# Optimization experiments

Hardware: AMD Instinct MI355X
Metric: run time of the kernel (lower is better)

## Reference

```python
import jax, jax.numpy as jnp
import numpy as np

N = 50000   # num_nodes
E = 600000  # num_edges
F = 128     # num_features
H = 128     # hidden_dim
C = 40      # num_classes


def setup_inputs() -> dict:
    key = jax.random.key(0)
    ks = jax.random.split(key, 8)
    x = jax.random.normal(ks[0], (N, F), dtype=jnp.float32)
    edge_index = jax.random.randint(ks[1], (2, E), 0, N, dtype=jnp.int64)
    # alpha predictors (torch inits these to zero; use small random so alpha is non-trivial)
    aw1 = jax.random.normal(ks[2], (F, 1), dtype=jnp.float32) * 0.01
    ab1 = jnp.zeros((1,), dtype=jnp.float32)
    aw2 = jax.random.normal(ks[3], (H, 1), dtype=jnp.float32) * 0.01
    ab2 = jnp.zeros((1,), dtype=jnp.float32)
    # projection weights, torch layout [out, in], xavier-uniform-ish scale
    W1 = jax.random.normal(ks[4], (H, F), dtype=jnp.float32) * np.sqrt(2.0 / (F + H))
    b1 = jnp.zeros((H,), dtype=jnp.float32)
    W2 = jax.random.normal(ks[5], (C, H), dtype=jnp.float32) * np.sqrt(2.0 / (H + C))
    b2 = jnp.zeros((C,), dtype=jnp.float32)
    return {"x": x, "edge_index": edge_index, "aw1": aw1, "ab1": ab1,
            "W1": W1, "b1": b1, "aw2": aw2, "ab2": ab2, "W2": W2, "b2": b2}


def _gso_edges(edge_index):
    """Add self loops and compute GCN-normalized edge weights: D^-1/2 (A+I) D^-1/2."""
    loops = jnp.arange(N, dtype=edge_index.dtype)
    row = jnp.concatenate([edge_index[0], loops])
    col = jnp.concatenate([edge_index[1], loops])
    deg = jax.ops.segment_sum(jnp.ones(row.shape, dtype=jnp.float32), row, num_segments=N)
    dinv = jnp.where(deg > 0, jax.lax.rsqrt(deg), 0.0)
    w = dinv[row] * dinv[col]  # [E+N]
    return row, col, w


def _layer(x, row, col, w, aw, ab, Wt, b, activate):
    alpha = jax.nn.sigmoid(x @ aw + ab)                              # [N,1]
    z_lp = jax.ops.segment_sum(w[:, None] * x[col], row, num_segments=N)  # S_LP @ x
    z_hp = x - z_lp                                                  # S_HP = I - S_LP
    z = alpha * z_lp + (1.0 - alpha) * z_hp
    out = z @ Wt.T + b
    return jax.nn.relu(out) if activate else out


def reference(x, edge_index, aw1, ab1, W1, b1, aw2, ab2, W2, b2):
    row, col, w = _gso_edges(edge_index)
    h = _layer(x, row, col, w, aw1, ab1, W1, b1, True)   # dropout p in eval = identity
    out = _layer(h, row, col, w, aw2, ab2, W2, b2, False)
    return out
```

## Files before the change

kernel.cpp:

```cpp
#include <hip/hip_runtime.h>

#define F 128
#define BIN_CAP 6144

typedef _Float16 half8 __attribute__((ext_vector_type(8)));
typedef float f32x4 __attribute__((ext_vector_type(4)));

__device__ inline unsigned int f2_to_h2(float a, float b) {
    union { _Float16 h[2]; unsigned int u; } c;
    c.h[0] = (_Float16)a; c.h[1] = (_Float16)b;
    return c.u;
}
__device__ inline float2 h2_to_f2(unsigned int v) {
    union { unsigned int u; _Float16 h[2]; } c; c.u = v;
    return make_float2((float)c.h[0], (float)c.h[1]);
}

__global__ void zc_kernel(int* __restrict__ binCnt, const float* __restrict__ x,
                          const float* __restrict__ W1, const float* __restrict__ W2,
                          unsigned int* __restrict__ xf, unsigned int* __restrict__ w1f,
                          unsigned int* __restrict__ w2f, int nx) {
    int i = blockIdx.x * blockDim.x + threadIdx.x;
    if (i < 256) { binCnt[i] = 0; return; }
    int j = i - 256;
    if (j < nx) {
        float2 v = ((const float2*)x)[j];
        xf[j] = f2_to_h2(v.x, v.y);
    } else if (j < nx + (F * F / 2)) {
        int k = j - nx;
        float2 v = ((const float2*)W1)[k];
        w1f[k] = f2_to_h2(v.x, v.y);
    } else if (j < nx + (F * F / 2) + (48 * F / 2)) {
        int k = j - nx - (F * F / 2);
        int m = k >> 6;
        if (m < 40) {
            float2 v = ((const float2*)W2)[k];
            w2f[k] = f2_to_h2(v.x, v.y);
        } else {
            w2f[k] = 0u;
        }
    }
}

__global__ __launch_bounds__(256) void binning_kernel(const int* __restrict__ row,
                                                      const int* __restrict__ col,
                                                      int* __restrict__ binCnt,
                                                      unsigned int* __restrict__ binned, int e) {
    __shared__ int cnt1[256], base[256], cnt2[256];
    int chunk0 = blockIdx.x * 4096;
    cnt1[threadIdx.x] = 0;
    cnt2[threadIdx.x] = 0;
    __syncthreads();
    #pragma unroll
    for (int k = 0; k < 16; ++k) {
        int i = chunk0 + k * 256 + threadIdx.x;
        if (i < e) atomicAdd(&cnt1[row[i] >> 8], 1);
    }
    __syncthreads();
    int c = cnt1[threadIdx.x];
    if (c > 0) base[threadIdx.x] = atomicAdd(&binCnt[threadIdx.x], c);
    __syncthreads();
    #pragma unroll
    for (int k = 0; k < 16; ++k) {
        int i = chunk0 + k * 256 + threadIdx.x;
        if (i < e) {
            int r = row[i], cl = col[i];
            int b = r >> 8;
            int rk = atomicAdd(&cnt2[b], 1);
            int pos = base[b] + rk;
            if (pos < BIN_CAP)
                binned[(size_t)b * BIN_CAP + pos] = ((unsigned int)(r & 255) << 24) | (unsigned int)cl;
        }
    }
}

__global__ __launch_bounds__(256) void finalize_kernel(const int* __restrict__ binCnt,
                                                       const unsigned int* __restrict__ binned,
                                                       int* __restrict__ rowStart,
                                                       float* __restrict__ dinv,
                                                       int* __restrict__ csr_col,
                                                       int n, int nb) {
    __shared__ int tmp[256], lc[256], lo[256], lc2[256];
    __shared__ int sBase, sSz;
    int tid = threadIdx.x;
    int b = blockIdx.x;
    int v = (tid < nb) ? binCnt[tid] : 0;
    tmp[tid] = v;
    __syncthreads();
    #pragma unroll
    for (int off = 1; off < 256; off <<= 1) {
        int t = (tid >= off) ? tmp[tid - off] : 0;
        __syncthreads();
        tmp[tid] += t;
        __syncthreads();
    }
    if (tid == b) { sBase = tmp[b] - v; sSz = v; }
    lc[tid] = 0;
    lc2[tid] = 0;
    __syncthreads();
    int base = sBase, sz = sSz;
    for (int i = tid; i < sz; i += 256) {
        unsigned int pv = binned[(size_t)b * BIN_CAP + i];
        atomicAdd(&lc[pv >> 24], 1);
    }
    __syncthreads();
    int cv = lc[tid];
    tmp[tid] = cv;
    __syncthreads();
    #pragma unroll
    for (int off = 1; off < 256; off <<= 1) {
        int t = (tid >= off) ? tmp[tid - off] : 0;
        __syncthreads();
        tmp[tid] += t;
        __syncthreads();
    }
    int myLo = tmp[tid] - cv;
    lo[tid] = myLo;
    int rowId = (b << 8) + tid;
    if (rowId < n) {
        rowStart[rowId] = base + myLo;
        dinv[rowId] = rsqrtf((float)(cv + 1));
    }
    if (tid == 0 && b == nb - 1) rowStart[n] = base + sz;
    __syncthreads();
    for (int i = tid; i < sz; i += 256) {
        unsigned int pv = binned[(size_t)b * BIN_CAP + i];
        int rl = pv >> 24;
        int rk = atomicAdd(&lc2[rl], 1);
        csr_col[base + lo[rl] + rk] = (int)(pv & 0xFFFFFFu);
    }
}

__global__ void gather_kernel(const unsigned int* __restrict__ featf,
                              const int* __restrict__ rowStart, const int* __restrict__ csr_col,
                              const float* __restrict__ dinv, const float* __restrict__ aw,
                              const float* __restrict__ ab, unsigned int* __restrict__ zf, int n) {
    int wid = (blockIdx.x * blockDim.x + threadIdx.x) >> 6;
    int lane = threadIdx.x & 63;
    if (wid >= n) return;
    float2 xv = h2_to_f2(featf[(size_t)wid * 64 + lane]);
    float2 awv = ((const float2*)aw)[lane];
    float s = xv.x * awv.x + xv.y * awv.y;
    #pragma unroll
    for (int off = 32; off > 0; off >>= 1) s += __shfl_down(s, off);
    s = __shfl(s, 0);
    float a = 1.0f / (1.0f + expf(-(s + ab[0])));
    float dr = dinv[wid];
    float2 acc;
    acc.x = dr * dr * xv.x;
    acc.y = dr * dr * xv.y;
    int j = rowStart[wid], en = rowStart[wid + 1];
    for (; j + 3 < en; j += 4) {
        int c0 = csr_col[j], c1 = csr_col[j + 1], c2 = csr_col[j + 2], c3 = csr_col[j + 3];
        float w0 = dr * dinv[c0], w1 = dr * dinv[c1], w2 = dr * dinv[c2], w3 = dr * dinv[c3];
        float2 f0 = h2_to_f2(featf[(size_t)c0 * 64 + lane]);
        float2 f1 = h2_to_f2(featf[(size_t)c1 * 64 + lane]);
        float2 f2 = h2_to_f2(featf[(size_t)c2 * 64 + lane]);
        float2 f3 = h2_to_f2(featf[(size_t)c3 * 64 + lane]);
        acc.x += w0 * f0.x; acc.y += w0 * f0.y;
        acc.x += w1 * f1.x; acc.y += w1 * f1.y;
        acc.x += w2 * f2.x; acc.y += w2 * f2.y;
        acc.x += w3 * f3.x; acc.y += w3 * f3.y;
    }
    for (; j < en; ++j) {
        int c0 = csr_col[j];
        float w0 = dr * dinv[c0];
        float2 f0 = h2_to_f2(featf[(size_t)c0 * 64 + lane]);
        acc.x += w0 * f0.x; acc.y += w0 * f0.y;
    }
    float ca = 1.0f - a, cb = 2.0f * a - 1.0f;
    zf[(size_t)wid * 64 + lane] = f2_to_h2(ca * xv.x + cb * acc.x, ca * xv.y + cb * acc.y);
}

__global__ __launch_bounds__(256) void mfma_dense_kernel(
    const _Float16* __restrict__ zf, const _Float16* __restrict__ w1f,
    const float* __restrict__ b1, const float* __restrict__ aw2,
    const float* __restrict__ ab2, const _Float16* __restrict__ w2f,
    _Float16* __restrict__ yf, float* __restrict__ alpha2, int n) {
    __shared__ _Float16 hs[64 * F];
    int wv = threadIdx.x >> 6;
    int l = threadIdx.x & 63;
    int lr = l & 15;
    int kg = l >> 4;
    int node0 = blockIdx.x * 64;

    int arow = node0 + wv * 16 + lr;
    bool rowok = arow < n;
    half8 afr[4];
    half8 hzero = {0, 0, 0, 0, 0, 0, 0, 0};
    #pragma unroll
    for (int ks = 0; ks < 4; ++ks) {
        afr[ks] = rowok ? *(const half8*)(zf + (size_t)arow * F + ks * 32 + kg * 8) : hzero;
    }

    f32x4 acc[8];
    #pragma unroll
    for (int ct = 0; ct < 8; ++ct) {
        f32x4 a = {0.f, 0.f, 0.f, 0.f};
        #pragma unroll
        for (int ks = 0; ks < 4; ++ks) {
            half8 b = *(const half8*)(w1f + (size_t)(ct * 16 + lr) * F + ks * 32 + kg * 8);
            a = __builtin_amdgcn_mfma_f32_16x16x32_f16(afr[ks], b, a, 0, 0, 0);
        }
        acc[ct] = a;
    }

    float part[4] = {0.f, 0.f, 0.f, 0.f};
    #pragma unroll
    for (int ct = 0; ct < 8; ++ct) {
        int colc = ct * 16 + lr;
        float bv = b1[colc];
        float av = aw2[colc];
        #pragma unroll
        for (int r = 0; r < 4; ++r) {
            float h = fmaxf(acc[ct][r] + bv, 0.f);
            part[r] += h * av;
            int hrow = wv * 16 + kg * 4 + r;
            int byteoff = (hrow * 256 + colc * 2) ^ ((hrow & 7) << 4);
            *(_Float16*)((char*)hs + byteoff) = (_Float16)h;
        }
    }
    #pragma unroll
    for (int off = 1; off < 16; off <<= 1) {
        #pragma unroll
        for (int r = 0; r < 4; ++r) part[r] += __shfl_xor(part[r], off);
    }
    if (lr == 0) {
        #pragma unroll
        for (int r = 0; r < 4; ++r) {
            int nd = node0 + wv * 16 + kg * 4 + r;
            if (nd < n) alpha2[nd] = 1.0f / (1.0f + expf(-(part[r] + ab2[0])));
        }
    }
    __syncthreads();

    int hrow = wv * 16 + lr;
    half8 a2[4];
    #pragma unroll
    for (int ks = 0; ks < 4; ++ks) {
        int byteoff = (hrow * 256 + (ks * 32 + kg * 8) * 2) ^ ((hrow & 7) << 4);
        a2[ks] = *(const half8*)((char*)hs + byteoff);
    }
    #pragma unroll
    for (int ct = 0; ct < 3; ++ct) {
        f32x4 a = {0.f, 0.f, 0.f, 0.f};
        #pragma unroll
        for (int ks = 0; ks < 4; ++ks) {
            half8 b = *(const half8*)(w2f + (size_t)(ct * 16 + lr) * F + ks * 32 + kg * 8);
            a = __builtin_amdgcn_mfma_f32_16x16x32_f16(a2[ks], b, a, 0, 0, 0);
        }
        int colc = ct * 16 + lr;
        if (colc < 40) {
            #pragma unroll
            for (int r = 0; r < 4; ++r) {
                int nd = node0 + wv * 16 + kg * 4 + r;
                if (nd < n) yf[(size_t)nd * 40 + colc] = (_Float16)a[r];
            }
        }
    }
}

__global__ void gather40_kernel(const _Float16* __restrict__ yf,
                                const int* __restrict__ rowStart, const int* __restrict__ csr_col,
                                const float* __restrict__ dinv, const float* __restrict__ alpha,
                                const float* __restrict__ bias, float* __restrict__ out, int n) {
    int node = blockIdx.x * 8 + threadIdx.x / 40;
    int lane = threadIdx.x % 40;
    if (node >= n) return;
    float yv = (float)yf[(size_t)node * 40 + lane];
    float dr = dinv[node];
    float acc = dr * dr * yv;
    int j = rowStart[node], en = rowStart[node + 1];
    for (; j + 3 < en; j += 4) {
        int c0 = csr_col[j], c1 = csr_col[j + 1], c2 = csr_col[j + 2], c3 = csr_col[j + 3];
        acc += dr * dinv[c0] * (float)yf[(size_t)c0 * 40 + lane];
        acc += dr * dinv[c1] * (float)yf[(size_t)c1 * 40 + lane];
        acc += dr * dinv[c2] * (float)yf[(size_t)c2 * 40 + lane];
        acc += dr * dinv[c3] * (float)yf[(size_t)c3 * 40 + lane];
    }
    for (; j < en; ++j) {
        int c0 = csr_col[j];
        acc += dr * dinv[c0] * (float)yf[(size_t)c0 * 40 + lane];
    }
    float a = alpha[node];
    out[(size_t)node * 40 + lane] = (1.0f - a) * yv + (2.0f * a - 1.0f) * acc + bias[lane];
}

extern "C" void kernel_launch(void* const* d_in, const int* in_sizes, int n_in,
                              void* d_out, int out_size, void* d_ws, size_t ws_size,
                              hipStream_t stream) {
    const float* x   = (const float*)d_in[0];
    const int*   ei  = (const int*)d_in[1];
    const float* aw1 = (const float*)d_in[2];
    const float* ab1 = (const float*)d_in[3];
    const float* W1  = (const float*)d_in[4];
    const float* b1  = (const float*)d_in[5];
    const float* aw2 = (const float*)d_in[6];
    const float* ab2 = (const float*)d_in[7];
    const float* W2  = (const float*)d_in[8];
    const float* b2  = (const float*)d_in[9];
    float* out = (float*)d_out;

    int n = in_sizes[0] / F;
    int e = in_sizes[1] / 2;
    const int* row = ei;
    const int* col = ei + e;
    int nb = (n + 255) >> 8;

    char* p = (char*)d_ws;
    auto alloc = [&](size_t bytes) { char* q = p; p += (bytes + 15) & ~(size_t)15; return q; };
    int*   binCnt   = (int*)alloc(256 * 4);
    int*   rowStart = (int*)alloc((size_t)(n + 2) * 4);
    float* dinv     = (float*)alloc((size_t)n * 4);
    unsigned int* binned = (unsigned int*)alloc((size_t)nb * BIN_CAP * 4);
    int*   csr_col  = (int*)alloc((size_t)e * 4);
    unsigned int* w1f = (unsigned int*)alloc((size_t)F * F * 2);
    unsigned int* w2f = (unsigned int*)alloc((size_t)48 * F * 2);
    unsigned int* xf  = (unsigned int*)alloc((size_t)n * 64 * 4);
    unsigned int* zf  = (unsigned int*)alloc((size_t)n * 64 * 4);
    _Float16* yfbuf = (_Float16*)alloc((size_t)n * 40 * 2);
    float* alpha2   = (float*)alloc((size_t)n * 4);

    int nx = n * 64;

    int nzc = 256 + nx + (F * F / 2) + (48 * F / 2);
    zc_kernel<<<(nzc + 255) / 256, 256, 0, stream>>>(binCnt, x, W1, W2, xf, w1f, w2f, nx);

    binning_kernel<<<(e + 4095) / 4096, 256, 0, stream>>>(row, col, binCnt, binned, e);
    finalize_kernel<<<nb, 256, 0, stream>>>(binCnt, binned, rowStart, dinv, csr_col, n, nb);

    gather_kernel<<<(n + 3) / 4, 256, 0, stream>>>(xf, rowStart, csr_col, dinv,
                                                   aw1, ab1, zf, n);

    int gblk = (n + 63) / 64;
    mfma_dense_kernel<<<gblk, 256, 0, stream>>>((const _Float16*)zf, (const _Float16*)w1f,
                                                b1, aw2, ab2, (const _Float16*)w2f,
                                                yfbuf, alpha2, n);

    gather40_kernel<<<(n + 7) / 8, 320, 0, stream>>>(yfbuf, rowStart, csr_col, dinv,
                                                     alpha2, b2, out, n);
}
```

Measured before the change: 128.6 us.

## Split layer-1 gather into two feature-half passes and precompute alpha in convert

The conversion kernel now computes the layer-1 alpha gate per node while converting x to fp16, storing it in a new buffer. The layer-1 gather is split into two launches, each handling half of the feature columns with 32 lanes per node. Each pass touches only half of every neighbour row, so its working set is smaller and may fit the cache better for the random neighbour reads. The cost is re-reading the CSR indices and dinv twice and paying an extra kernel launch.

```diff
diff --git a/kernel.cpp b/kernel.cpp
--- a/kernel.cpp
+++ b/kernel.cpp
@@ -16,30 +16,42 @@
     return make_float2((float)c.h[0], (float)c.h[1]);
 }
 
-__global__ void zc_kernel(int* __restrict__ binCnt, const float* __restrict__ x,
-                          const float* __restrict__ W1, const float* __restrict__ W2,
-                          unsigned int* __restrict__ xf, unsigned int* __restrict__ w1f,
-                          unsigned int* __restrict__ w2f, int nx) {
-    int i = blockIdx.x * blockDim.x + threadIdx.x;
-    if (i < 256) { binCnt[i] = 0; return; }
-    int j = i - 256;
-    if (j < nx) {
-        float2 v = ((const float2*)x)[j];
-        xf[j] = f2_to_h2(v.x, v.y);
-    } else if (j < nx + (F * F / 2)) {
-        int k = j - nx;
-        float2 v = ((const float2*)W1)[k];
-        w1f[k] = f2_to_h2(v.x, v.y);
-    } else if (j < nx + (F * F / 2) + (48 * F / 2)) {
-        int k = j - nx - (F * F / 2);
-        int m = k >> 6;
-        if (m < 40) {
-            float2 v = ((const float2*)W2)[k];
-            w2f[k] = f2_to_h2(v.x, v.y);
+__global__ __launch_bounds__(256) void convert_kernel(
+    const float* __restrict__ x, const float* __restrict__ aw1, const float* __restrict__ ab1,
+    const float* __restrict__ W1, const float* __restrict__ W2,
+    unsigned int* __restrict__ xf, float* __restrict__ alpha1,
+    unsigned int* __restrict__ w1f, unsigned int* __restrict__ w2f,
+    int* __restrict__ binCnt, int n, int nodeBlocks) {
+    if (blockIdx.x >= nodeBlocks) {
+        int i = (blockIdx.x - nodeBlocks) * 256 + threadIdx.x;
+        if (i < 256) {
+            binCnt[i] = 0;
+        } else if (i < 256 + F * F / 2) {
+            int j = i - 256;
+            float2 v = ((const float2*)W1)[j];
+            w1f[j] = f2_to_h2(v.x, v.y);
         } else {
-            w2f[k] = 0u;
-        }
-    }
+            int j = i - 256 - F * F / 2;
+            int m = j >> 6;
+            if (m < 40) {
+                float2 v = ((const float2*)W2)[j];
+                w2f[j] = f2_to_h2(v.x, v.y);
+            } else {
+                w2f[j] = 0u;
+            }
+        }
+        return;
+    }
+    int wid = blockIdx.x * 4 + (threadIdx.x >> 6);
+    int lane = threadIdx.x & 63;
+    if (wid >= n) return;
+    float2 xv = ((const float2*)(x + (size_t)wid * F))[lane];
+    float2 awv = ((const float2*)aw1)[lane];
+    float s = xv.x * awv.x + xv.y * awv.y;
+    #pragma unroll
+    for (int off = 32; off > 0; off >>= 1) s += __shfl_down(s, off);
+    if (lane == 0) alpha1[wid] = 1.0f / (1.0f + expf(-(s + ab1[0])));
+    xf[(size_t)wid * 64 + lane] = f2_to_h2(xv.x, xv.y);
 }
 
 __global__ __launch_bounds__(256) void binning_kernel(const int* __restrict__ row,
@@ -131,32 +143,27 @@
     }
 }
 
-__global__ void gather_kernel(const unsigned int* __restrict__ featf,
-                              const int* __restrict__ rowStart, const int* __restrict__ csr_col,
-                              const float* __restrict__ dinv, const float* __restrict__ aw,
-                              const float* __restrict__ ab, unsigned int* __restrict__ zf, int n) {
-    int wid = (blockIdx.x * blockDim.x + threadIdx.x) >> 6;
-    int lane = threadIdx.x & 63;
-    if (wid >= n) return;
-    float2 xv = h2_to_f2(featf[(size_t)wid * 64 + lane]);
-    float2 awv = ((const float2*)aw)[lane];
-    float s = xv.x * awv.x + xv.y * awv.y;
-    #pragma unroll
-    for (int off = 32; off > 0; off >>= 1) s += __shfl_down(s, off);
-    s = __shfl(s, 0);
-    float a = 1.0f / (1.0f + expf(-(s + ab[0])));
-    float dr = dinv[wid];
+__global__ __launch_bounds__(256) void gather_half_kernel(
+    const unsigned int* __restrict__ xf, const int* __restrict__ rowStart,
+    const int* __restrict__ csr_col, const float* __restrict__ dinv,
+    const float* __restrict__ alpha1, unsigned int* __restrict__ zf, int n, int half) {
+    int grp = (blockIdx.x * 256 + threadIdx.x) >> 5;
+    int ui = threadIdx.x & 31;
+    if (grp >= n) return;
+    size_t rowBase = (size_t)grp * 64 + half * 32;
+    float2 xv = h2_to_f2(xf[rowBase + ui]);
+    float dr = dinv[grp];
     float2 acc;
     acc.x = dr * dr * xv.x;
     acc.y = dr * dr * xv.y;
-    int j = rowStart[wid], en = rowStart[wid + 1];
+    int j = rowStart[grp], en = rowStart[grp + 1];
     for (; j + 3 < en; j += 4) {
         int c0 = csr_col[j], c1 = csr_col[j + 1], c2 = csr_col[j + 2], c3 = csr_col[j + 3];
         float w0 = dr * dinv[c0], w1 = dr * dinv[c1], w2 = dr * dinv[c2], w3 = dr * dinv[c3];
-        float2 f0 = h2_to_f2(featf[(size_t)c0 * 64 + lane]);
-        float2 f1 = h2_to_f2(featf[(size_t)c1 * 64 + lane]);
-        float2 f2 = h2_to_f2(featf[(size_t)c2 * 64 + lane]);
-        float2 f3 = h2_to_f2(featf[(size_t)c3 * 64 + lane]);
+        float2 f0 = h2_to_f2(xf[(size_t)c0 * 64 + half * 32 + ui]);
+        float2 f1 = h2_to_f2(xf[(size_t)c1 * 64 + half * 32 + ui]);
+        float2 f2 = h2_to_f2(xf[(size_t)c2 * 64 + half * 32 + ui]);
+        float2 f3 = h2_to_f2(xf[(size_t)c3 * 64 + half * 32 + ui]);
         acc.x += w0 * f0.x; acc.y += w0 * f0.y;
         acc.x += w1 * f1.x; acc.y += w1 * f1.y;
         acc.x += w2 * f2.x; acc.y += w2 * f2.y;
@@ -165,11 +172,12 @@
     for (; j < en; ++j) {
         int c0 = csr_col[j];
         float w0 = dr * dinv[c0];
-        float2 f0 = h2_to_f2(featf[(size_t)c0 * 64 + lane]);
+        float2 f0 = h2_to_f2(xf[(size_t)c0 * 64 + half * 32 + ui]);
         acc.x += w0 * f0.x; acc.y += w0 * f0.y;
     }
+    float a = alpha1[grp];
     float ca = 1.0f - a, cb = 2.0f * a - 1.0f;
-    zf[(size_t)wid * 64 + lane] = f2_to_h2(ca * xv.x + cb * acc.x, ca * xv.y + cb * acc.y);
+    zf[rowBase + ui] = f2_to_h2(ca * xv.x + cb * acc.x, ca * xv.y + cb * acc.y);
 }
 
 __global__ __launch_bounds__(256) void mfma_dense_kernel(
@@ -312,6 +320,7 @@
     int*   binCnt   = (int*)alloc(256 * 4);
     int*   rowStart = (int*)alloc((size_t)(n + 2) * 4);
     float* dinv     = (float*)alloc((size_t)n * 4);
+    float* alpha1   = (float*)alloc((size_t)n * 4);
     unsigned int* binned = (unsigned int*)alloc((size_t)nb * BIN_CAP * 4);
     int*   csr_col  = (int*)alloc((size_t)e * 4);
     unsigned int* w1f = (unsigned int*)alloc((size_t)F * F * 2);
@@ -321,16 +330,19 @@
     _Float16* yfbuf = (_Float16*)alloc((size_t)n * 40 * 2);
     float* alpha2   = (float*)alloc((size_t)n * 4);
 
-    int nx = n * 64;
-
-    int nzc = 256 + nx + (F * F / 2) + (48 * F / 2);
-    zc_kernel<<<(nzc + 255) / 256, 256, 0, stream>>>(binCnt, x, W1, W2, xf, w1f, w2f, nx);
+    int nodeBlocks = (n + 3) / 4;
+    int tailBlocks = (256 + F * F / 2 + 48 * F / 2 + 255) / 256;
+    convert_kernel<<<nodeBlocks + tailBlocks, 256, 0, stream>>>(
+        x, aw1, ab1, W1, W2, xf, alpha1, w1f, w2f, binCnt, n, nodeBlocks);
 
     binning_kernel<<<(e + 4095) / 4096, 256, 0, stream>>>(row, col, binCnt, binned, e);
     finalize_kernel<<<nb, 256, 0, stream>>>(binCnt, binned, rowStart, dinv, csr_col, n, nb);
 
-    gather_kernel<<<(n + 3) / 4, 256, 0, stream>>>(xf, rowStart, csr_col, dinv,
-                                                   aw1, ab1, zf, n);
+    int gHalfBlk = (n * 32 + 255) / 256;
+    gather_half_kernel<<<gHalfBlk, 256, 0, stream>>>(xf, rowStart, csr_col, dinv, alpha1,
+                                                     zf, n, 0);
+    gather_half_kernel<<<gHalfBlk, 256, 0, stream>>>(xf, rowStart, csr_col, dinv, alpha1,
+                                                     zf, n, 1);
 
     int gblk = (n + 63) / 64;
     mfma_dense_kernel<<<gblk, 256, 0, stream>>>((const _Float16*)zf, (const _Float16*)w1f,
```

Result: slower. 144.5 us (+12.4%).
